# Performance work log

Hardware: AMD Instinct MI355X
Metric: run time of the kernel (lower is better)

## Reference

```python
import jax, jax.numpy as jnp
import numpy as np

NUM_HEADS = 12
DIM_HEADS = 64
DIM = 768
D_H = NUM_HEADS * DIM_HEADS  # 768
B, N = 8, 1024


def setup_inputs() -> dict:
    key = jax.random.key(0)
    k1, k2, k3, k4 = jax.random.split(key, 4)
    img = jax.random.normal(k1, (B, N, DIM), dtype=jnp.float32)
    # torch nn.Linear stores weight as [out_features, in_features]
    W_qkv = jax.random.normal(k2, (3 * D_H, DIM), dtype=jnp.float32) * (DIM ** -0.5)
    W_fc = jax.random.normal(k3, (DIM, D_H), dtype=jnp.float32) * (D_H ** -0.5)
    b_fc = jax.random.normal(k4, (DIM,), dtype=jnp.float32) * 0.01
    return {"img": img, "W_qkv": W_qkv, "W_fc": W_fc, "b_fc": b_fc}


def reference(img, W_qkv, W_fc, b_fc):
    b, n, _ = img.shape
    # qkv projection (no bias): [B, N, 3*D_h]
    qkv = jnp.einsum('bnd,ed->bne', img, W_qkv)
    # reshape to [B, N, H, 3*dh], move heads forward -> [B, H, N, 3*dh]
    qkv = qkv.reshape(b, n, NUM_HEADS, 3 * DIM_HEADS).transpose(0, 2, 1, 3)
    q, k, v = jnp.split(qkv, 3, axis=-1)  # each [B, H, N, dh]
    # NOTE: original code MULTIPLIES by sqrt(dim_heads) (unusual, kept faithful)
    scale = jnp.sqrt(jnp.float32(DIM_HEADS))
    scores = jnp.einsum('bhqd,bhkd->bhqk', q, k) * scale  # [B, H, N, N]
    attn = jax.nn.softmax(scores, axis=-1)
    out = jnp.einsum('bhqk,bhkd->bhqd', attn, v)  # [B, H, N, dh]
    # merge heads -> [B, N, D_h], then output projection (dropout is identity at eval)
    out = out.transpose(0, 2, 1, 3).reshape(b, n, D_H)
    return jnp.einsum('bne,de->bnd', out, W_fc) + b_fc
```

## Files before the change

kernel.cpp:

```cpp
#include <hip/hip_runtime.h>
#include <math.h>


typedef __attribute__((ext_vector_type(8))) short short8;
typedef __attribute__((ext_vector_type(4))) float f32x4;

#define MFMA(a, b, c) __builtin_amdgcn_mfma_f32_16x16x32_bf16((a), (b), (c), 0, 0, 0)

#define GLDS16(gp, lp) \
  __builtin_amdgcn_global_load_lds((__attribute__((address_space(1))) const void*)(gp), \
                                   (__attribute__((address_space(3))) void*)(lp), 16, 0, 0)

__device__ __forceinline__ unsigned short f2bf(float x) {
  unsigned u = __builtin_bit_cast(unsigned, x);
  return (unsigned short)((u + 0x7FFFu + ((u >> 16) & 1u)) >> 16);
}
__device__ __forceinline__ float bf2f(unsigned short h) {
  unsigned u = ((unsigned)h) << 16;
  return __builtin_bit_cast(float, u);
}

__global__ __launch_bounds__(256)
void k_split(const float* __restrict__ x, short* __restrict__ h,
             short* __restrict__ l, int n8)
{
  const int i = blockIdx.x * 256 + threadIdx.x;
  if (i >= n8) return;
  float4 a = ((const float4*)x)[2 * i];
  float4 b = ((const float4*)x)[2 * i + 1];
  float v[8] = {a.x, a.y, a.z, a.w, b.x, b.y, b.z, b.w};
  short8 hh, ll;
#pragma unroll
  for (int e = 0; e < 8; ++e) {
    unsigned short hi = f2bf(v[e]);
    hh[e] = (short)hi;
    ll[e] = (short)f2bf(v[e] - bf2f(hi));
  }
  ((short8*)h)[i] = hh;
  ((short8*)l)[i] = ll;
}

template <int EPI>
__global__ __launch_bounds__(256, 3)
void k_gemm(const short* __restrict__ AH, const short* __restrict__ AL,
            const short* __restrict__ WH, const short* __restrict__ WL,
            const float* __restrict__ bias, float* __restrict__ Cf,
            short* __restrict__ qkH, short* __restrict__ qkL,
            short* __restrict__ vTH, short* __restrict__ vTL,
            int Ndim, int K)
{
  __shared__ __align__(16) short As[128 * 64];
  __shared__ __align__(16) short Ws[128 * 64];

  const int tid = threadIdx.x, lane = tid & 63, w = tid >> 6;
  const int wm = w >> 1, wn = w & 1;
  const int fr = lane & 15, g = lane >> 4;
  const int bm = blockIdx.x * 128, bn = blockIdx.y * 128;

  const int l3 = lane >> 3;
  const int ssrc = (lane & 7) ^ l3;

  const f32x4 zero4 = {0.f, 0.f, 0.f, 0.f};
  f32x4 acc[4][4];
#pragma unroll
  for (int i = 0; i < 4; ++i)
#pragma unroll
    for (int j = 0; j < 4; ++j) acc[i][j] = zero4;

  const short* aplane = (ssrc < 4) ? AH : AL;
  const short* wplane = (ssrc < 4) ? WH : WL;
  const int scol = (ssrc & 3) * 8;

  const int nk = K >> 5;
  for (int kt = 0; kt < nk; ++kt) {
    const int k0 = kt << 5;
    __syncthreads();
#pragma unroll
    for (int c = 0; c < 8; ++c) {
      const int gidx = w * 8 + c;
      const int ch = gidx & 15;
      const int row = ch * 8 + l3;
      if (gidx < 16) {
        GLDS16(aplane + (size_t)(bm + row) * K + k0 + scol, &As[ch * 512]);
      } else {
        GLDS16(wplane + (size_t)(bn + row) * K + k0 + scol, &Ws[ch * 512]);
      }
    }
    __syncthreads();

    short8 aH[4], aL[4], bH[4], bL[4];
#pragma unroll
    for (int i = 0; i < 4; ++i) {
      const int ra = wm * 64 + i * 16 + fr;
      aH[i] = *(const short8*)&As[ra * 64 + ((g ^ (ra & 7)) * 8)];
      aL[i] = *(const short8*)&As[ra * 64 + (((4 + g) ^ (ra & 7)) * 8)];
      const int rb = wn * 64 + i * 16 + fr;
      bH[i] = *(const short8*)&Ws[rb * 64 + ((g ^ (rb & 7)) * 8)];
      bL[i] = *(const short8*)&Ws[rb * 64 + (((4 + g) ^ (rb & 7)) * 8)];
    }
#pragma unroll
    for (int i = 0; i < 4; ++i)
#pragma unroll
      for (int j = 0; j < 4; ++j) {
        acc[i][j] = MFMA(aH[i], bH[j], acc[i][j]);
        acc[i][j] = MFMA(aH[i], bL[j], acc[i][j]);
        acc[i][j] = MFMA(aL[i], bH[j], acc[i][j]);
      }
  }

  const int row0 = bm + wm * 64 + g * 4;
  if constexpr (EPI == 0) {
    const int colbase = bn + wn * 64;
    const int species = (colbase >> 6) % 3;
    const int head = colbase / 192;
    if (species < 2) {
      const int qkcol0 = head * 128 + species * 64 + fr;
#pragma unroll
      for (int i = 0; i < 4; ++i)
#pragma unroll
        for (int j = 0; j < 4; ++j) {
          const size_t base = (size_t)(row0 + i * 16) * 1536 + qkcol0 + j * 16;
#pragma unroll
          for (int r = 0; r < 4; ++r) {
            const float x = acc[i][j][r];
            const unsigned short hi = f2bf(x);
            qkH[base + (size_t)r * 1536] = (short)hi;
            qkL[base + (size_t)r * 1536] = (short)f2bf(x - bf2f(hi));
          }
        }
    } else {
#pragma unroll
      for (int i = 0; i < 4; ++i) {
        const int n0 = row0 + i * 16;
        const int b = n0 >> 10, n = n0 & 1023;
#pragma unroll
        for (int j = 0; j < 4; ++j) {
          const int dv = j * 16 + fr;
          short4 h4, l4;
#pragma unroll
          for (int r = 0; r < 4; ++r) {
            const float x = acc[i][j][r];
            const unsigned short hi = f2bf(x);
            ((short*)&h4)[r] = (short)hi;
            ((short*)&l4)[r] = (short)f2bf(x - bf2f(hi));
          }
          const size_t vidx = ((size_t)(b * 12 + head) * 64 + dv) * 1024 + n;
          *(short4*)&vTH[vidx] = h4;
          *(short4*)&vTL[vidx] = l4;
        }
      }
    }
  } else {
    const int col0 = bn + wn * 64 + fr;
    float bj[4];
#pragma unroll
    for (int j = 0; j < 4; ++j) bj[j] = bias[col0 + j * 16];
#pragma unroll
    for (int i = 0; i < 4; ++i)
#pragma unroll
      for (int j = 0; j < 4; ++j) {
        const int row = row0 + i * 16, col = col0 + j * 16;
#pragma unroll
        for (int r = 0; r < 4; ++r)
          Cf[(size_t)(row + r) * Ndim + col] = acc[i][j][r] + bj[j];
      }
  }
}

__global__ __launch_bounds__(256, 3)
void k_attn(const short* __restrict__ qkH, const short* __restrict__ qkL,
            const short* __restrict__ vTH, const short* __restrict__ vTL,
            short* __restrict__ attH, short* __restrict__ attL)
{
  __shared__ __align__(16) short Kls[2][64 * 64];
  __shared__ __align__(16) short Vls[2][64 * 64];
  __shared__ __align__(16) short Ps[4][32][72];

  const int tid = threadIdx.x, lane = tid & 63, w = tid >> 6;
  const int fr = lane & 15, g = lane >> 4;
  const int l3 = lane >> 3;
  const int ssrc = (lane & 7) ^ l3;

  const int bid = blockIdx.x;
  const int lg = (bid & 7) * 96 + (bid >> 3);
  const int qt = lg & 7;
  const int bh = lg >> 3;
  const int b = bh / 12, h = bh - b * 12;

  const f32x4 zero4 = {0.f, 0.f, 0.f, 0.f};

  short8 qH[2][2], qL[2][2];
#pragma unroll
  for (int i = 0; i < 2; ++i) {
    const int row = qt * 128 + w * 32 + i * 16 + fr;
    const size_t base = (size_t)(b * 1024 + row) * 1536 + h * 128 + g * 8;
#pragma unroll
    for (int ks = 0; ks < 2; ++ks) {
      qH[i][ks] = *(const short8*)&qkH[base + ks * 32];
      qL[i][ks] = *(const short8*)&qkL[base + ks * 32];
    }
  }

  f32x4 O[2][4];
  float mrun[2][4], lrun[2][4];
#pragma unroll
  for (int i = 0; i < 2; ++i)
#pragma unroll
    for (int r = 0; r < 4; ++r) { mrun[i][r] = -INFINITY; lrun[i][r] = 0.f; }
#pragma unroll
  for (int i = 0; i < 2; ++i)
#pragma unroll
    for (int nf = 0; nf < 4; ++nf) O[i][nf] = zero4;

  short8 ones;
#pragma unroll
  for (int e = 0; e < 8; ++e) ones[e] = (short)0x3F80;

  const short* kplane = (w & 1) ? qkL : qkH;
  const short* vplane = (w & 1) ? vTL : vTH;
  short* dstA = (w < 2) ? &Kls[w & 1][0] : &Vls[w & 1][0];

  for (int kt = 0; kt < 16; ++kt) {
    const int kv0 = kt * 64;
    __syncthreads();
#pragma unroll
    for (int c = 0; c < 8; ++c) {
      const int row = c * 8 + l3;
      const short* src = (w < 2)
        ? kplane + (size_t)(b * 1024 + kv0 + row) * 1536 + h * 128 + 64 + ssrc * 8
        : vplane + ((size_t)bh * 64 + row) * 1024 + kv0 + ssrc * 8;
      GLDS16(src, dstA + c * 512);
    }
    __syncthreads();

    f32x4 S[2][4];
#pragma unroll
    for (int i = 0; i < 2; ++i)
#pragma unroll
      for (int nf = 0; nf < 4; ++nf) S[i][nf] = zero4;
#pragma unroll
    for (int nf = 0; nf < 4; ++nf) {
      const int rk = nf * 16 + fr;
#pragma unroll
      for (int ks = 0; ks < 2; ++ks) {
        const int t = g + 4 * ks;
        const int sidx = rk * 64 + ((t ^ (rk & 7)) * 8);
        short8 kbh = *(const short8*)&Kls[0][sidx];
        short8 kbl = *(const short8*)&Kls[1][sidx];
#pragma unroll
        for (int i = 0; i < 2; ++i) {
          S[i][nf] = MFMA(qH[i][ks], kbh, S[i][nf]);
          S[i][nf] = MFMA(qH[i][ks], kbl, S[i][nf]);
          S[i][nf] = MFMA(qL[i][ks], kbh, S[i][nf]);
        }
      }
    }

    float al[2][4];
#pragma unroll
    for (int i = 0; i < 2; ++i) {
      float tl[4];
#pragma unroll
      for (int r = 0; r < 4; ++r)
        tl[r] = fmaxf(fmaxf(S[i][0][r], S[i][1][r]), fmaxf(S[i][2][r], S[i][3][r]));
#pragma unroll
      for (int off = 1; off < 16; off <<= 1)
#pragma unroll
        for (int r = 0; r < 4; ++r) tl[r] = fmaxf(tl[r], __shfl_xor(tl[r], off));
#pragma unroll
      for (int r = 0; r < 4; ++r) {
        const float mn = fmaxf(mrun[i][r], tl[r] * 8.f);
        al[i][r] = __expf(mrun[i][r] - mn);
        mrun[i][r] = mn;
#pragma unroll
        for (int nf = 0; nf < 4; ++nf) {
          const float p = __expf(fmaf(S[i][nf][r], 8.f, -mn));
          Ps[w][i * 16 + g * 4 + r][nf * 16 + fr] = (short)f2bf(p);
        }
      }
    }

    short8 pa[2][2];
#pragma unroll
    for (int i = 0; i < 2; ++i)
#pragma unroll
      for (int ks = 0; ks < 2; ++ks)
        pa[i][ks] = *(const short8*)&Ps[w][i * 16 + fr][ks * 32 + g * 8];

#pragma unroll
    for (int i = 0; i < 2; ++i) {
      f32x4 rs = MFMA(pa[i][0], ones, zero4);
      rs = MFMA(pa[i][1], ones, rs);
#pragma unroll
      for (int r = 0; r < 4; ++r)
        lrun[i][r] = lrun[i][r] * al[i][r] + rs[r];
#pragma unroll
      for (int nf = 0; nf < 4; ++nf)
#pragma unroll
        for (int r = 0; r < 4; ++r) O[i][nf][r] *= al[i][r];
    }

#pragma unroll
    for (int nf = 0; nf < 4; ++nf) {
      const int rd = nf * 16 + fr;
#pragma unroll
      for (int ks = 0; ks < 2; ++ks) {
        const int t = g + 4 * ks;
        const int sidx = rd * 64 + ((t ^ (rd & 7)) * 8);
        short8 vbh = *(const short8*)&Vls[0][sidx];
        short8 vbl = *(const short8*)&Vls[1][sidx];
#pragma unroll
        for (int i = 0; i < 2; ++i) {
          O[i][nf] = MFMA(pa[i][ks], vbh, O[i][nf]);
          O[i][nf] = MFMA(pa[i][ks], vbl, O[i][nf]);
        }
      }
    }
  }

#pragma unroll
  for (int i = 0; i < 2; ++i) {
    const size_t rowbase = (size_t)(b * 1024 + qt * 128 + w * 32 + i * 16 + g * 4);
#pragma unroll
    for (int r = 0; r < 4; ++r) {
      const float inv = 1.f / lrun[i][r];
#pragma unroll
      for (int nf = 0; nf < 4; ++nf) {
        const float v = O[i][nf][r] * inv;
        const size_t idx = (rowbase + r) * 768 + h * 64 + nf * 16 + fr;
        const unsigned short hi = f2bf(v);
        attH[idx] = (short)hi;
        attL[idx] = (short)f2bf(v - bf2f(hi));
      }
    }
  }
}


extern "C" void kernel_launch(void* const* d_in, const int* in_sizes, int n_in,
                              void* d_out, int out_size, void* d_ws, size_t ws_size,
                              hipStream_t stream)
{
  const float* img  = (const float*)d_in[0];
  const float* Wqkv = (const float*)d_in[1];
  const float* Wfc  = (const float*)d_in[2];
  const float* bfc  = (const float*)d_in[3];
  float* outp = (float*)d_out;

  char* ws = (char*)d_ws;
  short* qkH   = (short*)(ws);
  short* qkL   = (short*)(ws + 25165824);
  short* vTH   = (short*)(ws + 50331648);
  short* vTL   = (short*)(ws + 62914560);
  short* imgH  = (short*)(ws + 75497472);
  short* imgL  = (short*)(ws + 88080384);
  short* WqkvH = (short*)(ws + 100663296);
  short* WqkvL = (short*)(ws + 104202240);
  short* WfcH  = (short*)(ws + 107741184);
  short* WfcL  = (short*)(ws + 108920832);
  short* attH  = imgH;
  short* attL  = imgL;

  k_split<<<3072, 256, 0, stream>>>(img,  imgH,  imgL,  786432);
  k_split<<<864,  256, 0, stream>>>(Wqkv, WqkvH, WqkvL, 221184);
  k_split<<<288,  256, 0, stream>>>(Wfc,  WfcH,  WfcL,  73728);
  k_gemm<0><<<dim3(64, 18), dim3(256), 0, stream>>>(
      imgH, imgL, WqkvH, WqkvL, nullptr, nullptr,
      qkH, qkL, vTH, vTL, 2304, 768);
  k_attn<<<dim3(768), dim3(256), 0, stream>>>(qkH, qkL, vTH, vTL, attH, attL);
  k_gemm<1><<<dim3(64, 6), dim3(256), 0, stream>>>(
      attH, attL, WfcH, WfcL, bfc, outp,
      nullptr, nullptr, nullptr, nullptr, 768, 768);
}
```

Measured before the change: 304.6 us.

## Add double-buffered 128x192 QKV GEMM kernel with one head per block

Replaces the templated QKV projection GEMM with a dedicated kernel of 384 threads and 128x192 tiles, so each block column covers exactly one head's q, k and v. LDS is double-buffered and the next K-slice's global-to-LDS loads are interleaved with the MFMA phases, using barriers and s_setprio to raise the priority of the matrix work. The goal is to hide load latency and cut the per-tile epilogue branching. The cost is more LDS per block (about 80 KB), which may limit occupancy, plus extra barriers per K step.

Measured after the change: 313.0 us. +2.8%, slower.

```diff
diff --git a/kernel.cpp b/kernel.cpp
--- a/kernel.cpp
+++ b/kernel.cpp
@@ -40,13 +40,139 @@
   ((short8*)l)[i] = ll;
 }
 
-template <int EPI>
+__global__ __launch_bounds__(384, 3)
+void k_gemm8(const short* __restrict__ AH, const short* __restrict__ AL,
+             const short* __restrict__ WH, const short* __restrict__ WL,
+             short* __restrict__ qkH, short* __restrict__ qkL,
+             short* __restrict__ vTH, short* __restrict__ vTL)
+{
+  __shared__ __align__(16) short As[2][128 * 64];
+  __shared__ __align__(16) short Bs[2][192 * 64];
+
+  const int tid = threadIdx.x, lane = tid & 63, w = tid >> 6;
+  const int wm = w / 3, wn = w - wm * 3;
+  const int fr = lane & 15, g = lane >> 4;
+  const int l3 = lane >> 3;
+  const int ssrc = (lane & 7) ^ l3;
+  const int bm = blockIdx.x * 128, bn = blockIdx.y * 192;
+  const int by = blockIdx.y;
+
+  const short* aplane = (ssrc < 4) ? AH : AL;
+  const short* wplane = (ssrc < 4) ? WH : WL;
+  const int scol = (ssrc & 3) * 8;
+  const bool isA = (w < 2);
+
+  const f32x4 zero4 = {0.f, 0.f, 0.f, 0.f};
+  f32x4 acc[4][4];
+#pragma unroll
+  for (int i = 0; i < 4; ++i)
+#pragma unroll
+    for (int j = 0; j < 4; ++j) acc[i][j] = zero4;
+
+  auto stage = [&](int buf, int kt, int c) {
+    const int k0 = kt << 5;
+    if (isA) {
+      const int ca = w * 8 + c;
+      GLDS16(aplane + (size_t)(bm + ca * 8 + l3) * 768 + k0 + scol, &As[buf][ca * 512]);
+    } else {
+      const int cb = (w - 2) * 6 + c;
+      GLDS16(wplane + (size_t)(bn + cb * 8 + l3) * 768 + k0 + scol, &Bs[buf][cb * 512]);
+    }
+  };
+
+#pragma unroll
+  for (int c = 0; c < 8; ++c)
+    if (c < (isA ? 8 : 6)) stage(0, 0, c);
+  __syncthreads();
+
+  for (int kt = 0; kt < 24; ++kt) {
+    const int cur = kt & 1, nxt = cur ^ 1;
+    const bool more = (kt < 23);
+
+    short8 bHf[4], bLf[4];
+#pragma unroll
+    for (int j = 0; j < 4; ++j) {
+      const int rb = wn * 64 + j * 16 + fr;
+      bHf[j] = *(const short8*)&Bs[cur][rb * 64 + ((g ^ (rb & 7)) * 8)];
+      bLf[j] = *(const short8*)&Bs[cur][rb * 64 + (((4 + g) ^ (rb & 7)) * 8)];
+    }
+
+#pragma unroll
+    for (int p = 0; p < 4; ++p) {
+      const int ra = wm * 64 + p * 16 + fr;
+      short8 aHf = *(const short8*)&As[cur][ra * 64 + ((g ^ (ra & 7)) * 8)];
+      short8 aLf = *(const short8*)&As[cur][ra * 64 + (((4 + g) ^ (ra & 7)) * 8)];
+
+      if (more) {
+        if (p == 0) {
+          stage(nxt, kt + 1, 0); stage(nxt, kt + 1, 1); stage(nxt, kt + 1, 2);
+          if (isA) stage(nxt, kt + 1, 3);
+        } else if (p == 1) {
+          if (isA) { stage(nxt, kt + 1, 4); stage(nxt, kt + 1, 5);
+                     stage(nxt, kt + 1, 6); stage(nxt, kt + 1, 7); }
+          else     { stage(nxt, kt + 1, 3); stage(nxt, kt + 1, 4);
+                     stage(nxt, kt + 1, 5); }
+        }
+      }
+
+      __builtin_amdgcn_s_barrier();
+      __builtin_amdgcn_s_setprio(1);
+#pragma unroll
+      for (int j = 0; j < 4; ++j) {
+        acc[p][j] = MFMA(aHf, bHf[j], acc[p][j]);
+        acc[p][j] = MFMA(aHf, bLf[j], acc[p][j]);
+        acc[p][j] = MFMA(aLf, bHf[j], acc[p][j]);
+      }
+      __builtin_amdgcn_s_setprio(0);
+      if (p < 3) __builtin_amdgcn_s_barrier();
+    }
+    __syncthreads();
+  }
+
+  if (wn < 2) {
+#pragma unroll
+    for (int i = 0; i < 4; ++i)
+#pragma unroll
+      for (int j = 0; j < 4; ++j) {
+        const int row = bm + wm * 64 + i * 16 + g * 4;
+        const int col = by * 128 + wn * 64 + j * 16 + fr;
+        const size_t base = (size_t)row * 1536 + col;
+#pragma unroll
+        for (int r = 0; r < 4; ++r) {
+          const float x = acc[i][j][r];
+          const unsigned short hi = f2bf(x);
+          qkH[base + (size_t)r * 1536] = (short)hi;
+          qkL[base + (size_t)r * 1536] = (short)f2bf(x - bf2f(hi));
+        }
+      }
+  } else {
+#pragma unroll
+    for (int i = 0; i < 4; ++i) {
+      const int n0 = bm + wm * 64 + i * 16 + g * 4;
+      const int b = n0 >> 10, n = n0 & 1023;
+#pragma unroll
+      for (int j = 0; j < 4; ++j) {
+        const int dv = j * 16 + fr;
+        short4 h4, l4;
+#pragma unroll
+        for (int r = 0; r < 4; ++r) {
+          const float x = acc[i][j][r];
+          const unsigned short hi = f2bf(x);
+          ((short*)&h4)[r] = (short)hi;
+          ((short*)&l4)[r] = (short)f2bf(x - bf2f(hi));
+        }
+        const size_t vidx = ((size_t)(b * 12 + by) * 64 + dv) * 1024 + n;
+        *(short4*)&vTH[vidx] = h4;
+        *(short4*)&vTL[vidx] = l4;
+      }
+    }
+  }
+}
+
 __global__ __launch_bounds__(256, 3)
 void k_gemm(const short* __restrict__ AH, const short* __restrict__ AL,
             const short* __restrict__ WH, const short* __restrict__ WL,
             const float* __restrict__ bias, float* __restrict__ Cf,
-            short* __restrict__ qkH, short* __restrict__ qkL,
-            short* __restrict__ vTH, short* __restrict__ vTL,
             int Ndim, int K)
 {
   __shared__ __align__(16) short As[128 * 64];
@@ -109,62 +235,19 @@
   }
 
   const int row0 = bm + wm * 64 + g * 4;
-  if constexpr (EPI == 0) {
-    const int colbase = bn + wn * 64;
-    const int species = (colbase >> 6) % 3;
-    const int head = colbase / 192;
-    if (species < 2) {
-      const int qkcol0 = head * 128 + species * 64 + fr;
-#pragma unroll
-      for (int i = 0; i < 4; ++i)
-#pragma unroll
-        for (int j = 0; j < 4; ++j) {
-          const size_t base = (size_t)(row0 + i * 16) * 1536 + qkcol0 + j * 16;
-#pragma unroll
-          for (int r = 0; r < 4; ++r) {
-            const float x = acc[i][j][r];
-            const unsigned short hi = f2bf(x);
-            qkH[base + (size_t)r * 1536] = (short)hi;
-            qkL[base + (size_t)r * 1536] = (short)f2bf(x - bf2f(hi));
-          }
-        }
-    } else {
-#pragma unroll
-      for (int i = 0; i < 4; ++i) {
-        const int n0 = row0 + i * 16;
-        const int b = n0 >> 10, n = n0 & 1023;
-#pragma unroll
-        for (int j = 0; j < 4; ++j) {
-          const int dv = j * 16 + fr;
-          short4 h4, l4;
-#pragma unroll
-          for (int r = 0; r < 4; ++r) {
-            const float x = acc[i][j][r];
-            const unsigned short hi = f2bf(x);
-            ((short*)&h4)[r] = (short)hi;
-            ((short*)&l4)[r] = (short)f2bf(x - bf2f(hi));
-          }
-          const size_t vidx = ((size_t)(b * 12 + head) * 64 + dv) * 1024 + n;
-          *(short4*)&vTH[vidx] = h4;
-          *(short4*)&vTL[vidx] = l4;
-        }
-      }
-    }
-  } else {
-    const int col0 = bn + wn * 64 + fr;
-    float bj[4];
-#pragma unroll
-    for (int j = 0; j < 4; ++j) bj[j] = bias[col0 + j * 16];
-#pragma unroll
-    for (int i = 0; i < 4; ++i)
-#pragma unroll
-      for (int j = 0; j < 4; ++j) {
-        const int row = row0 + i * 16, col = col0 + j * 16;
-#pragma unroll
-        for (int r = 0; r < 4; ++r)
-          Cf[(size_t)(row + r) * Ndim + col] = acc[i][j][r] + bj[j];
-      }
-  }
+  const int col0 = bn + wn * 64 + fr;
+  float bj[4];
+#pragma unroll
+  for (int j = 0; j < 4; ++j) bj[j] = bias[col0 + j * 16];
+#pragma unroll
+  for (int i = 0; i < 4; ++i)
+#pragma unroll
+    for (int j = 0; j < 4; ++j) {
+      const int row = row0 + i * 16, col = col0 + j * 16;
+#pragma unroll
+      for (int r = 0; r < 4; ++r)
+        Cf[(size_t)(row + r) * Ndim + col] = acc[i][j][r] + bj[j];
+    }
 }
 
 __global__ __launch_bounds__(256, 3)
@@ -364,11 +447,9 @@
   k_split<<<3072, 256, 0, stream>>>(img,  imgH,  imgL,  786432);
   k_split<<<864,  256, 0, stream>>>(Wqkv, WqkvH, WqkvL, 221184);
   k_split<<<288,  256, 0, stream>>>(Wfc,  WfcH,  WfcL,  73728);
-  k_gemm<0><<<dim3(64, 18), dim3(256), 0, stream>>>(
-      imgH, imgL, WqkvH, WqkvL, nullptr, nullptr,
-      qkH, qkL, vTH, vTL, 2304, 768);
+  k_gemm8<<<dim3(64, 12), dim3(384), 0, stream>>>(
+      imgH, imgL, WqkvH, WqkvL, qkH, qkL, vTH, vTL);
   k_attn<<<dim3(768), dim3(256), 0, stream>>>(qkH, qkL, vTH, vTL, attH, attL);
-  k_gemm<1><<<dim3(64, 6), dim3(256), 0, stream>>>(
-      attH, attL, WfcH, WfcL, bfc, outp,
-      nullptr, nullptr, nullptr, nullptr, 768, 768);
-}
+  k_gemm<<<dim3(64, 6), dim3(256), 0, stream>>>(
+      attH, attL, WfcH, WfcL, bfc, outp, 768, 768);
+}
```
